# Performance work log

Measured on AMD Instinct MI355X. Metric: run time of the kernel, lower is better.

## Reference

```python
import jax, jax.numpy as jnp
import numpy as np

NEG_SLOPE = 0.2  # PyG GATConv default negative_slope
N_GRAPHS = 128


def gat_conv(x, src, dst, w, a_src, a_dst, b):
    """PyG GATConv (v1), concat=True. x:[N,F], src/dst:[E] (self-loops included),
    w:[F,H*C], a_src/a_dst:[H,C], b:[H*C]."""
    N = x.shape[0]
    H, C = a_src.shape
    h = (x @ w).reshape(N, H, C)                      # [N,H,C]
    e = (h * a_src).sum(-1)[src] + (h * a_dst).sum(-1)[dst]  # [E,H]
    e = jnp.where(e > 0, e, NEG_SLOPE * e)            # leaky_relu
    m = jax.ops.segment_max(e, dst, num_segments=N)   # per-dst softmax max
    ex = jnp.exp(e - m[dst])
    s = jax.ops.segment_sum(ex, dst, num_segments=N)
    alpha = ex / (s[dst] + 1e-16)                     # [E,H]
    out = jax.ops.segment_sum(h[src] * alpha[:, :, None], dst, num_segments=N)
    return out.reshape(N, H * C) + b


def pool(x, batch, num_graphs):
    """concat(global_mean_pool, global_max_pool)."""
    ones = jnp.ones((x.shape[0],), x.dtype)
    cnt = jax.ops.segment_sum(ones, batch, num_segments=num_graphs)
    mean = jax.ops.segment_sum(x, batch, num_segments=num_graphs) / jnp.maximum(cnt, 1.0)[:, None]
    mx = jax.ops.segment_max(x, batch, num_segments=num_graphs)
    return jnp.concatenate([mean, mx], axis=-1)


def setup_inputs() -> dict:
    key = jax.random.key(0)
    ks = jax.random.split(key, 30)
    N, E, G = 100000, 800000, N_GRAPHS
    F_in, H, C = 260, 4, 64
    HC = H * C  # 256

    def lin(k, i, o):
        return (jax.random.normal(k, (i, o), jnp.float32) * (1.0 / np.sqrt(i)))

    def att(k):
        return jax.random.normal(k, (H, C), jnp.float32) * 0.1

    return {
        "x": jax.random.normal(ks[0], (N, F_in), jnp.float32),
        "edge_index": jax.random.randint(ks[1], (2, E), 0, N),
        "batch": jnp.sort(jax.random.randint(ks[2], (N,), 0, G)),
        "gat1_w": lin(ks[3], F_in, HC), "gat1_as": att(ks[4]), "gat1_ad": att(ks[5]),
        "gat1_b": jnp.zeros((HC,), jnp.float32),
        "lin1_w": lin(ks[6], HC, C), "lin1_b": jnp.zeros((C,), jnp.float32),
        "gat2_w": lin(ks[7], C, HC), "gat2_as": att(ks[8]), "gat2_ad": att(ks[9]),
        "gat2_b": jnp.zeros((HC,), jnp.float32),
        "lin2_w": lin(ks[10], HC, C), "lin2_b": jnp.zeros((C,), jnp.float32),
        "sum_w": lin(ks[11], 4 * C, 2 * C), "sum_b": jnp.zeros((2 * C,), jnp.float32),
        "sh1_w": lin(ks[12], 2 * C, C), "sh1_b": jnp.zeros((C,), jnp.float32),
        "sh2_w": lin(ks[13], C, C), "sh2_b": jnp.zeros((C,), jnp.float32),
        "sh3_w": lin(ks[14], C, C), "sh3_b": jnp.zeros((C,), jnp.float32),
        "reg_w": lin(ks[15], C, 32), "reg_b": jnp.zeros((32,), jnp.float32),
    }


def reference(x, edge_index, batch,
              gat1_w, gat1_as, gat1_ad, gat1_b, lin1_w, lin1_b,
              gat2_w, gat2_as, gat2_ad, gat2_b, lin2_w, lin2_b,
              sum_w, sum_b, sh1_w, sh1_b, sh2_w, sh2_b, sh3_w, sh3_b,
              reg_w, reg_b):
    N = x.shape[0]
    loop = jnp.arange(N)
    src = jnp.concatenate([edge_index[0], loop])  # add_self_loops=True
    dst = jnp.concatenate([edge_index[1], loop])

    h = gat_conv(x, src, dst, gat1_w, gat1_as, gat1_ad, gat1_b)
    h = jax.nn.selu(h @ lin1_w + lin1_b)
    x1 = pool(h, batch, N_GRAPHS)                 # [G, 2C]

    h = gat_conv(h, src, dst, gat2_w, gat2_as, gat2_ad, gat2_b)
    h = jax.nn.selu(h @ lin2_w + lin2_b)
    x2 = pool(h, batch, N_GRAPHS)                 # [G, 2C]

    z = jnp.concatenate([x1, x2], axis=-1) @ sum_w + sum_b
    z = jax.nn.selu(z @ sh1_w + sh1_b)
    z = jax.nn.selu(z @ sh2_w + sh2_b)
    z = jax.nn.selu(z @ sh3_w + sh3_b)
    return z @ reg_w + reg_b                      # [G, 32]
```

## Files before the change

### kernel.cpp

```cpp
#include <hip/hip_runtime.h>
#include <hip/hip_bf16.h>
#include <cstdint>

#define NEG_SLOPE 0.2f
#define HEADS 4
#define CH 64
#define HC 256
#define F_IN 260
#define KPAD1 320
#define NGRAPH 128

typedef __attribute__((ext_vector_type(8))) short bf16x8;
typedef __attribute__((ext_vector_type(4))) float f32x4;

__device__ __forceinline__ float seluf(float x){
    const float sc=1.0507009873554805f, al=1.6732632423543772f;
    return x>0.f ? sc*x : sc*al*(__expf(x)-1.f);
}
__device__ __forceinline__ unsigned fenc(float x){
    unsigned u=__float_as_uint(x);
    return (u&0x80000000u)? ~u : (u|0x80000000u);
}
__device__ __forceinline__ float fdec(unsigned e){
    unsigned u = (e&0x80000000u)? (e&0x7fffffffu) : ~e;
    return __uint_as_float(u);
}
__device__ __forceinline__ float bf2f(unsigned short u){
    return __uint_as_float(((unsigned)u)<<16);
}
__device__ __forceinline__ unsigned short f2bf_raw(float x){
    unsigned u = __float_as_uint(x);
    unsigned rounded = u + 0x7fffu + ((u >> 16) & 1u);
    return (unsigned short)(rounded >> 16);
}
__device__ __forceinline__ void gload_lds16(const void* g, void* l){
    __builtin_amdgcn_global_load_lds(
        (const __attribute__((address_space(1))) void*)g,
        (__attribute__((address_space(3))) void*)l, 16, 0, 0);
}

__global__ void fill_u32_kernel(unsigned* p, unsigned v, int n){
    int i = blockIdx.x*blockDim.x + threadIdx.x;
    for (; i<n; i += gridDim.x*blockDim.x) p[i]=v;
}

__global__ void degree_kernel(const int* __restrict__ ei, int* __restrict__ deg, int E){
    int i = blockIdx.x*blockDim.x+threadIdx.x;
    for (; i<E; i+=gridDim.x*blockDim.x) atomicAdd(&deg[ei[E+i]], 1);
}

__global__ void scan_ph1(const int* __restrict__ deg, int* __restrict__ bsum, int N){
    __shared__ int sd[256];
    int base = blockIdx.x*1024;
    int t = threadIdx.x;
    int tot=0;
    for(int u=0;u<4;u++){ int i = base + t*4+u; tot += (i<N)? deg[i]:0; }
    sd[t]=tot; __syncthreads();
    for(int off=128; off; off>>=1){ if(t<off) sd[t]+=sd[t+off]; __syncthreads(); }
    if(t==0) bsum[blockIdx.x]=sd[0];
}
__global__ void scan_ph2(int* bsum, int nb, int* rowptr, int N, int E){
    if(threadIdx.x==0 && blockIdx.x==0){
        int run=0;
        for(int b=0;b<nb;b++){ int v=bsum[b]; bsum[b]=run; run+=v; }
        rowptr[N]=E;
    }
}
__global__ void scan_ph3(const int* __restrict__ deg, const int* __restrict__ bsum,
                         int* __restrict__ rowptr, int N){
    __shared__ int sd[256];
    int base = blockIdx.x*1024;
    int t = threadIdx.x;
    int v[4]; int tot=0;
    for(int u=0;u<4;u++){ int i=base+t*4+u; v[u] = (i<N)? deg[i]:0; tot+=v[u]; }
    sd[t]=tot; __syncthreads();
    for(int off=1; off<256; off<<=1){
        int add = (t>=off)? sd[t-off] : 0;
        __syncthreads();
        sd[t] += add;
        __syncthreads();
    }
    int pre = bsum[blockIdx.x] + ((t==0)?0: sd[t-1]);
    for(int u=0;u<4;u++){ int i=base+t*4+u; if(i<N){ rowptr[i]=pre; pre+=v[u]; } }
}

__global__ void scatter_kernel(const int* __restrict__ ei, const int* __restrict__ rowptr,
                               int* __restrict__ fil, int* __restrict__ col, int E){
    int i = blockIdx.x*blockDim.x+threadIdx.x;
    for(; i<E; i+=gridDim.x*blockDim.x){
        int s = ei[i], d = ei[E+i];
        int p = atomicAdd(&fil[d],1);
        col[rowptr[d]+p] = s;
    }
}

__global__ void cvt_x_kernel(const float* __restrict__ x, unsigned* __restrict__ xb, int N){
    int i = blockIdx.x*blockDim.x+threadIdx.x;
    int total = N*(KPAD1/2);
    for (; i<total; i+=gridDim.x*blockDim.x){
        int row = i/(KPAD1/2);
        int c2 = (i - row*(KPAD1/2))*2;
        float v0 = (c2   < F_IN) ? x[(size_t)row*F_IN + c2]   : 0.f;
        float v1 = (c2+1 < F_IN) ? x[(size_t)row*F_IN + c2+1] : 0.f;
        xb[i] = ((unsigned)f2bf_raw(v1) << 16) | f2bf_raw(v0);
    }
}

__global__ void cvt_wT_kernel(const float* __restrict__ w, __hip_bfloat16* __restrict__ wt,
                              int K, int NC, int Kpad){
    int i = blockIdx.x*blockDim.x+threadIdx.x;
    if (i >= NC*Kpad) return;
    int n = i / Kpad, k = i - n*Kpad;
    wt[i] = __float2bfloat16(k < K ? w[(size_t)k*NC + n] : 0.f);
}

template<int BN, int FS>
__global__ __launch_bounds__(512, 4) void mfma_gemm_kernel(
    const __hip_bfloat16* __restrict__ A, int Kpad,
    const __hip_bfloat16* __restrict__ Bt,
    const float* __restrict__ bias, int act,
    __hip_bfloat16* __restrict__ Cb,
    const float* __restrict__ asrc, const float* __restrict__ adst,
    float* __restrict__ ss, float* __restrict__ sdv,
    int M, int NC)
{
    constexpr int NF = BN/32;
    constexpr int WN = BN/2;
    constexpr int TP = WN + 8;
    __shared__ __align__(16) char lds[32768];

    int tid  = threadIdx.x;
    int lane = tid & 63;
    int w    = tid >> 6;
    int wr = w >> 1, wc = w & 1;
    int row0 = blockIdx.x * 128;
    int col0 = blockIdx.y * BN;
    int fr   = lane & 15;
    int koff = (lane >> 4) * 16;

    f32x4 acc[2][NF];
    #pragma unroll
    for (int i=0;i<2;i++)
        #pragma unroll
        for (int j=0;j<NF;j++) acc[i][j] = (f32x4){0.f,0.f,0.f,0.f};

    int lrow = lane >> 2;
    int lcolB = (lane & 3) * 16;
    int ktiles = Kpad >> 5;

    auto stage = [&](int kt, int pb){
        int k0b = kt*64;
        char* Asb = lds + pb*8192;
        char* Bsb = lds + 16384 + pb*(BN*64);
        {
            int gr = row0 + w*16 + lrow; if (gr > M-1) gr = M-1;
            gload_lds16((const char*)A + (size_t)gr*Kpad*2 + k0b + lcolB,
                        Asb + w*1024 + lrow*64 + lcolB);
        }
        if (w < BN/16){
            int gn = col0 + w*16 + lrow;
            gload_lds16((const char*)Bt + (size_t)gn*Kpad*2 + k0b + lcolB,
                        Bsb + w*1024 + lrow*64 + lcolB);
        }
    };

    stage(0, 0);
    __syncthreads();
    for (int kt=0; kt<ktiles; kt++){
        int pb = kt & 1;
        if (kt+1 < ktiles) stage(kt+1, pb^1);
        const char* Ab = lds + pb*8192;
        const char* Bb = lds + 16384 + pb*(BN*64);
        bf16x8 a[2], b[NF];
        a[0] = *(const bf16x8*)(Ab + (wr*32 +      fr)*64 + koff);
        a[1] = *(const bf16x8*)(Ab + (wr*32 + 16 + fr)*64 + koff);
        #pragma unroll
        for (int nt=0; nt<NF; nt++)
            b[nt] = *(const bf16x8*)(Bb + (wc*WN + nt*16 + fr)*64 + koff);
        #pragma unroll
        for (int mt=0; mt<2; mt++)
            #pragma unroll
            for (int nt=0; nt<NF; nt++)
                acc[mt][nt] = __builtin_amdgcn_mfma_f32_16x16x32_bf16(a[mt], b[nt], acc[mt][nt], 0, 0, 0);
        __syncthreads();
    }

    if (FS){
        float asv[NF], adv[NF];
        #pragma unroll
        for (int nt=0; nt<NF; nt++){
            int gc = col0 + wc*WN + nt*16 + fr;
            asv[nt] = asrc[gc];
            adv[nt] = adst[gc];
        }
        int head = (col0 + wc*WN) >> 6;
        #pragma unroll
        for (int mt=0; mt<2; mt++){
            #pragma unroll
            for (int r=0; r<4; r++){
                float ts=0.f, td=0.f;
                #pragma unroll
                for (int nt=0; nt<NF; nt++){
                    ts = fmaf(acc[mt][nt][r], asv[nt], ts);
                    td = fmaf(acc[mt][nt][r], adv[nt], td);
                }
                #pragma unroll
                for (int off=1; off<16; off<<=1){
                    ts += __shfl_xor(ts, off);
                    td += __shfl_xor(td, off);
                }
                if (fr==0){
                    int gr = row0 + wr*32 + mt*16 + (lane>>4)*4 + r;
                    if (gr < M){ ss[gr*4+head]=ts; sdv[gr*4+head]=td; }
                }
            }
        }
    }

    char* ct = lds + w*(16*TP*2);
    int c0 = col0 + wc*WN;
    #pragma unroll
    for (int mt=0; mt<2; mt++){
        #pragma unroll
        for (int nt=0; nt<NF; nt++){
            #pragma unroll
            for (int r=0; r<4; r++){
                float v = acc[mt][nt][r];
                if (bias) v += bias[c0 + nt*16 + fr];
                if (act)  v = seluf(v);
                int tr = (lane>>4)*4 + r;
                *(unsigned short*)(ct + tr*(TP*2) + (nt*16+fr)*2) = f2bf_raw(v);
            }
        }
        constexpr int CPR = WN/8;
        constexpr int RPP = 64/CPR;
        #pragma unroll
        for (int p=0; p<16/RPP; p++){
            int tr = p*RPP + lane/CPR;
            int ch = lane % CPR;
            int4 v = *(const int4*)(ct + tr*(TP*2) + ch*16);
            int gr = row0 + wr*32 + mt*16 + tr;
            if (gr < M)
                *(int4*)((char*)Cb + ((size_t)gr*NC + c0 + ch*8)*2) = v;
        }
    }
}

__global__ void softmax_prep_kernel(const float* __restrict__ ss, const float* __restrict__ sdv,
                                    const int* __restrict__ rowptr, const int* __restrict__ col,
                                    float2* __restrict__ minv, float* __restrict__ selfa, int N){
    int t = blockIdx.x*blockDim.x + threadIdx.x;
    int node = t >> 2;
    int h = t & 3;
    if (node >= N) return;
    float ad = sdv[node*4+h];
    float e0 = ss[node*4+h] + ad;
    e0 = e0>0.f ? e0 : NEG_SLOPE*e0;
    float m = e0, s = 1.f;
    int jb = rowptr[node], je = rowptr[node+1];
    for (int j=jb; j<je; j++){
        int sc = col[j];
        float e = ss[sc*4+h] + ad;
        e = e>0.f ? e : NEG_SLOPE*e;
        float mn = fmaxf(m, e);
        s = s*__expf(m-mn) + __expf(e-mn);
        m = mn;
    }
    float inv = 1.f / s;
    minv[node*4+h] = make_float2(m, inv);
    selfa[node*4+h] = __expf(e0-m)*inv;
}

__global__ void aggregate2_kernel(const __hip_bfloat16* __restrict__ h,
                                  const float* __restrict__ ss, const float* __restrict__ sdv,
                                  const float2* __restrict__ minv, const float* __restrict__ selfa,
                                  const int* __restrict__ rowptr, const int* __restrict__ col,
                                  const float* __restrict__ bias,
                                  __hip_bfloat16* __restrict__ outp, int N){
    int node = blockIdx.x*4 + (threadIdx.x>>6);
    if (node >= N) return;
    int lane = threadIdx.x & 63;
    int hh = lane >> 4;
    int c0 = (lane & 15) * 4;
    int idx = hh*64 + c0;
    const unsigned short* hp = (const unsigned short*)h;
    float ad = sdv[node*4+hh];
    float2 mi = minv[node*4+hh];
    float sa = selfa[node*4+hh];
    ushort4 hv = *(const ushort4*)(hp + (size_t)node*HC + idx);
    float a0 = sa*bf2f(hv.x), a1 = sa*bf2f(hv.y), a2 = sa*bf2f(hv.z), a3 = sa*bf2f(hv.w);
    int jb = rowptr[node], je = rowptr[node+1];
    int j = jb;
    for (; j+1 < je; j += 2){
        int sc0 = col[j], sc1 = col[j+1];
        float e0 = ss[sc0*4+hh] + ad;
        float e1 = ss[sc1*4+hh] + ad;
        e0 = e0>0.f ? e0 : NEG_SLOPE*e0;
        e1 = e1>0.f ? e1 : NEG_SLOPE*e1;
        float p0 = __expf(e0 - mi.x)*mi.y;
        float p1 = __expf(e1 - mi.x)*mi.y;
        ushort4 v0 = *(const ushort4*)(hp + (size_t)sc0*HC + idx);
        ushort4 v1 = *(const ushort4*)(hp + (size_t)sc1*HC + idx);
        a0 = fmaf(p0, bf2f(v0.x), a0); a1 = fmaf(p0, bf2f(v0.y), a1);
        a2 = fmaf(p0, bf2f(v0.z), a2); a3 = fmaf(p0, bf2f(v0.w), a3);
        a0 = fmaf(p1, bf2f(v1.x), a0); a1 = fmaf(p1, bf2f(v1.y), a1);
        a2 = fmaf(p1, bf2f(v1.z), a2); a3 = fmaf(p1, bf2f(v1.w), a3);
    }
    if (j < je){
        int sc0 = col[j];
        float e0 = ss[sc0*4+hh] + ad;
        e0 = e0>0.f ? e0 : NEG_SLOPE*e0;
        float p0 = __expf(e0 - mi.x)*mi.y;
        ushort4 v0 = *(const ushort4*)(hp + (size_t)sc0*HC + idx);
        a0 = fmaf(p0, bf2f(v0.x), a0); a1 = fmaf(p0, bf2f(v0.y), a1);
        a2 = fmaf(p0, bf2f(v0.z), a2); a3 = fmaf(p0, bf2f(v0.w), a3);
    }
    unsigned short* op = (unsigned short*)outp;
    size_t ob = (size_t)node*HC + idx;
    op[ob+0] = f2bf_raw(a0 + bias[idx+0]);
    op[ob+1] = f2bf_raw(a1 + bias[idx+1]);
    op[ob+2] = f2bf_raw(a2 + bias[idx+2]);
    op[ob+3] = f2bf_raw(a3 + bias[idx+3]);
}

__global__ void count_kernel(const int* __restrict__ batch, int* __restrict__ cnt, int N){
    int i = blockIdx.x*blockDim.x + threadIdx.x;
    if (i >= N) return;
    int lane = threadIdx.x & 63;
    int g = batch[i];
    int nfull = N & ~63;
    if (i < nfull){
        int g0 = __shfl(g, 0);
        if (__all(g==g0)){ if (lane==0) atomicAdd(&cnt[g0], 64); }
        else atomicAdd(&cnt[g], 1);
    } else {
        atomicAdd(&cnt[g], 1);
    }
}

__global__ void pool_kernel(const __hip_bfloat16* __restrict__ hs, const int* __restrict__ batch,
                            float* __restrict__ psum, unsigned* __restrict__ pmax, int N){
    int c = threadIdx.x & 63;
    int sub = threadIdx.x >> 6;
    int n0 = blockIdx.x*128 + sub*32;
    const unsigned short* hp = (const unsigned short*)hs;
    float s = 0.f, mx = -__builtin_inff();
    int cur = -1;
    for (int j=0; j<32; j++){
        int n = n0 + j;
        if (n >= N) break;
        int g = batch[n];
        if (g != cur){
            if (cur >= 0){
                atomicAdd(&psum[cur*64+c], s);
                atomicMax(&pmax[cur*64+c], fenc(mx));
            }
            cur = g; s = 0.f; mx = -__builtin_inff();
        }
        float v = bf2f(hp[(size_t)n*64 + c]);
        s += v; mx = fmaxf(mx, v);
    }
    if (cur >= 0){
        atomicAdd(&psum[cur*64+c], s);
        atomicMax(&pmax[cur*64+c], fenc(mx));
    }
}

__global__ void pool_final_kernel(const float* __restrict__ psum, const unsigned* __restrict__ pmax,
                                  const int* __restrict__ cnt, float* __restrict__ x, int G){
    int i = blockIdx.x*blockDim.x+threadIdx.x;
    if (i >= G*64) return;
    int g=i>>6, c=i&63;
    float cf = fmaxf((float)cnt[g], 1.f);
    x[g*128 + c] = psum[i]/cf;
    x[g*128 + 64 + c] = fdec(pmax[i]);
}

__global__ __launch_bounds__(128) void head_kernel(
    const float* __restrict__ x1, const float* __restrict__ x2,
    const float* __restrict__ sw, const float* __restrict__ sb,
    const float* __restrict__ w1, const float* __restrict__ b1,
    const float* __restrict__ w2, const float* __restrict__ b2,
    const float* __restrict__ w3, const float* __restrict__ b3,
    const float* __restrict__ rw, const float* __restrict__ rb,
    float* __restrict__ out)
{
    int g = blockIdx.x, t = threadIdx.x;
    __shared__ float v[256], z1[128], z2[64], z3[64], z4[64];
    v[t] = x1[g*128+t];
    v[128+t] = x2[g*128+t];
    __syncthreads();
    float a = sb[t];
    for(int k=0;k<256;k++) a = fmaf(v[k], sw[k*128+t], a);
    z1[t] = a;
    __syncthreads();
    if(t<64){
        float a2 = b1[t];
        for(int k=0;k<128;k++) a2 = fmaf(z1[k], w1[k*64+t], a2);
        z2[t] = seluf(a2);
    }
    __syncthreads();
    if(t<64){
        float a3 = b2[t];
        for(int k=0;k<64;k++) a3 = fmaf(z2[k], w2[k*64+t], a3);
        z3[t] = seluf(a3);
    }
    __syncthreads();
    if(t<64){
        float a4 = b3[t];
        for(int k=0;k<64;k++) a4 = fmaf(z3[k], w3[k*64+t], a4);
        z4[t] = seluf(a4);
    }
    __syncthreads();
    if(t<32){
        float a5 = rb[t];
        for(int k=0;k<64;k++) a5 = fmaf(z4[k], rw[k*32+t], a5);
        out[g*32+t] = a5;
    }
}

extern "C" void kernel_launch(void* const* d_in, const int* in_sizes, int n_in,
                              void* d_out, int out_size, void* d_ws, size_t ws_size,
                              hipStream_t stream)
{
    const float* x    = (const float*)d_in[0];
    const int*   ei   = (const int*)d_in[1];
    const int*   batch= (const int*)d_in[2];
    const float* g1w  = (const float*)d_in[3];
    const float* g1as = (const float*)d_in[4];
    const float* g1ad = (const float*)d_in[5];
    const float* g1b  = (const float*)d_in[6];
    const float* l1w  = (const float*)d_in[7];
    const float* l1b  = (const float*)d_in[8];
    const float* g2w  = (const float*)d_in[9];
    const float* g2as = (const float*)d_in[10];
    const float* g2ad = (const float*)d_in[11];
    const float* g2b  = (const float*)d_in[12];
    const float* l2w  = (const float*)d_in[13];
    const float* l2b  = (const float*)d_in[14];
    const float* sw   = (const float*)d_in[15];
    const float* sb   = (const float*)d_in[16];
    const float* s1w  = (const float*)d_in[17];
    const float* s1b  = (const float*)d_in[18];
    const float* s2w  = (const float*)d_in[19];
    const float* s2b  = (const float*)d_in[20];
    const float* s3w  = (const float*)d_in[21];
    const float* s3b  = (const float*)d_in[22];
    const float* rw   = (const float*)d_in[23];
    const float* rb   = (const float*)d_in[24];
    float* out = (float*)d_out;

    const int N = in_sizes[0] / F_IN;
    const int E = in_sizes[1] / 2;
    const int G = NGRAPH;

    char* ws = (char*)d_ws;
    size_t off = 0;
    auto alloc = [&](size_t bytes)->void*{
        void* p = ws + off;
        off += (bytes + 255) & ~(size_t)255;
        return p;
    };
    int* deg     = (int*)alloc((size_t)2*N*4);
    int* fil     = deg + N;
    int* rowptr  = (int*)alloc(((size_t)N+1)*4);
    int* col     = (int*)alloc((size_t)E*4);
    int* bsum    = (int*)alloc(1024);
    int* zpool   = (int*)alloc((size_t)(128 + 2*G*64)*4);
    int*   cnt = zpool;
    float* PS1 = (float*)(zpool + 128);
    float* PS2 = PS1 + G*64;
    unsigned* PM1 = (unsigned*)alloc((size_t)2*G*64*4);
    unsigned* PM2 = PM1 + G*64;
    float* X1    = (float*)alloc((size_t)G*128*4);
    float* X2    = (float*)alloc((size_t)G*128*4);
    __hip_bfloat16* Xb  = (__hip_bfloat16*)alloc((size_t)N*KPAD1*2);
    __hip_bfloat16* W1t = (__hip_bfloat16*)alloc((size_t)HC*KPAD1*2);
    __hip_bfloat16* L1t = (__hip_bfloat16*)alloc((size_t)CH*HC*2);
    __hip_bfloat16* W2t = (__hip_bfloat16*)alloc((size_t)HC*CH*2);
    __hip_bfloat16* L2t = (__hip_bfloat16*)alloc((size_t)CH*HC*2);
    __hip_bfloat16* Abf = (__hip_bfloat16*)alloc((size_t)N*HC*2);
    __hip_bfloat16* Bbf = (__hip_bfloat16*)alloc((size_t)N*HC*2);
    __hip_bfloat16* HSb = (__hip_bfloat16*)alloc((size_t)N*CH*2);
    float* SCS   = (float*)alloc((size_t)N*HEADS*4);
    float* SCD   = (float*)alloc((size_t)N*HEADS*4);
    float2* MNV  = (float2*)alloc((size_t)N*HEADS*8);
    float* SELFA = (float*)alloc((size_t)N*HEADS*4);
    (void)ws_size; (void)n_in; (void)out_size;

    const unsigned ENC_NEG_INF = 0x007FFFFFu;
    int nb = (N+1023)/1024;

    fill_u32_kernel<<<256,256,0,stream>>>((unsigned*)deg, 0u, 2*N);
    fill_u32_kernel<<<64,256,0,stream>>>((unsigned*)zpool, 0u, 128 + 2*G*64);
    fill_u32_kernel<<<64,256,0,stream>>>(PM1, ENC_NEG_INF, 2*G*64);

    degree_kernel<<<1024,256,0,stream>>>(ei, deg, E);
    scan_ph1<<<nb,256,0,stream>>>(deg, bsum, N);
    scan_ph2<<<1,64,0,stream>>>(bsum, nb, rowptr, N, E);
    scan_ph3<<<nb,256,0,stream>>>(deg, bsum, rowptr, N);
    scatter_kernel<<<1024,256,0,stream>>>(ei, rowptr, fil, col, E);

    cvt_x_kernel<<<2048,256,0,stream>>>(x, (unsigned*)Xb, N);
    cvt_wT_kernel<<<(HC*KPAD1+255)/256,256,0,stream>>>(g1w, W1t, F_IN, HC, KPAD1);
    cvt_wT_kernel<<<(CH*HC+255)/256,256,0,stream>>>(l1w, L1t, HC, CH, HC);
    cvt_wT_kernel<<<(HC*CH+255)/256,256,0,stream>>>(g2w, W2t, CH, HC, CH);
    cvt_wT_kernel<<<(CH*HC+255)/256,256,0,stream>>>(l2w, L2t, HC, CH, HC);

    int nodeBlocks = (N+3)/4;
    int prepBlocks = (N*4+255)/256;
    dim3 gA((N+127)/128, 2);
    dim3 gL((N+127)/128, 1);

    mfma_gemm_kernel<128,1><<<gA,512,0,stream>>>(Xb, KPAD1, W1t, nullptr, 0, Abf,
                                                 g1as, g1ad, SCS, SCD, N, HC);
    softmax_prep_kernel<<<prepBlocks,256,0,stream>>>(SCS, SCD, rowptr, col, MNV, SELFA, N);
    aggregate2_kernel<<<nodeBlocks,256,0,stream>>>(Abf, SCS, SCD, MNV, SELFA, rowptr, col, g1b, Bbf, N);
    mfma_gemm_kernel<64,0><<<gL,512,0,stream>>>(Bbf, HC, L1t, l1b, 1, HSb,
                                                nullptr, nullptr, nullptr, nullptr, N, CH);
    count_kernel<<<(N+255)/256,256,0,stream>>>(batch, cnt, N);
    pool_kernel<<<(N+127)/128,256,0,stream>>>(HSb, batch, PS1, PM1, N);
    pool_final_kernel<<<(G*64+255)/256,256,0,stream>>>(PS1, PM1, cnt, X1, G);

    mfma_gemm_kernel<128,1><<<gA,512,0,stream>>>(HSb, CH, W2t, nullptr, 0, Abf,
                                                 g2as, g2ad, SCS, SCD, N, HC);
    softmax_prep_kernel<<<prepBlocks,256,0,stream>>>(SCS, SCD, rowptr, col, MNV, SELFA, N);
    aggregate2_kernel<<<nodeBlocks,256,0,stream>>>(Abf, SCS, SCD, MNV, SELFA, rowptr, col, g2b, Bbf, N);
    mfma_gemm_kernel<64,0><<<gL,512,0,stream>>>(Bbf, HC, L2t, l2b, 1, HSb,
                                                nullptr, nullptr, nullptr, nullptr, N, CH);
    pool_kernel<<<(N+127)/128,256,0,stream>>>(HSb, batch, PS2, PM2, N);
    pool_final_kernel<<<(G*64+255)/256,256,0,stream>>>(PS2, PM2, cnt, X2, G);

    head_kernel<<<G,128,0,stream>>>(X1, X2, sw, sb, s1w, s1b, s2w, s2b, s3w, s3b, rw, rb, out);
}
```

Measured before the change: 524.0 us.

## Process four edges per wave in aggregate2 and shrink GEMM K padding

The aggregate2 kernel now splits each 64-lane wave into four edge slots. Each lane owns 16 contiguous channels and loads them as two 16-byte vectors, so four source rows are gathered concurrently. Partial sums are combined with cross-lane shuffles, and the output is written with wide vector stores. This is meant to raise memory-level parallelism on the irregular gathers and use wider loads and stores, at the cost of shuffle reductions and idle lanes when a node's degree is not a multiple of four. Separately, the first GEMM's K padding drops from 320 to 288 to cut wasted multiply work on the 260-wide input, which assumes 288 is still a multiple of that kernel's K tile.

```diff
diff --git a/kernel.cpp b/kernel.cpp
--- a/kernel.cpp
+++ b/kernel.cpp
@@ -7,10 +7,11 @@
 #define CH 64
 #define HC 256
 #define F_IN 260
-#define KPAD1 320
+#define KPAD1 288
 #define NGRAPH 128
 
 typedef __attribute__((ext_vector_type(8))) short bf16x8;
+typedef __attribute__((ext_vector_type(8))) unsigned short u16x8;
 typedef __attribute__((ext_vector_type(4))) float f32x4;
 
 __device__ __forceinline__ float seluf(float x){
@@ -280,47 +281,68 @@
     int node = blockIdx.x*4 + (threadIdx.x>>6);
     if (node >= N) return;
     int lane = threadIdx.x & 63;
-    int hh = lane >> 4;
-    int c0 = (lane & 15) * 4;
-    int idx = hh*64 + c0;
+    int s = lane >> 4;
+    int t = lane & 15;
+    int hh = t >> 2;
     const unsigned short* hp = (const unsigned short*)h;
+
     float ad = sdv[node*4+hh];
     float2 mi = minv[node*4+hh];
-    float sa = selfa[node*4+hh];
-    ushort4 hv = *(const ushort4*)(hp + (size_t)node*HC + idx);
-    float a0 = sa*bf2f(hv.x), a1 = sa*bf2f(hv.y), a2 = sa*bf2f(hv.z), a3 = sa*bf2f(hv.w);
+
+    float acc[16];
+    {
+        float sa = (s==0) ? selfa[node*4+hh] : 0.f;
+        const unsigned short* base = hp + (size_t)node*HC + t*16;
+        u16x8 v0 = *(const u16x8*)(base);
+        u16x8 v1 = *(const u16x8*)(base + 8);
+        #pragma unroll
+        for (int k=0;k<8;k++){
+            acc[k]   = sa * bf2f(v0[k]);
+            acc[8+k] = sa * bf2f(v1[k]);
+        }
+    }
+
     int jb = rowptr[node], je = rowptr[node+1];
-    int j = jb;
-    for (; j+1 < je; j += 2){
-        int sc0 = col[j], sc1 = col[j+1];
-        float e0 = ss[sc0*4+hh] + ad;
-        float e1 = ss[sc1*4+hh] + ad;
-        e0 = e0>0.f ? e0 : NEG_SLOPE*e0;
-        e1 = e1>0.f ? e1 : NEG_SLOPE*e1;
-        float p0 = __expf(e0 - mi.x)*mi.y;
-        float p1 = __expf(e1 - mi.x)*mi.y;
-        ushort4 v0 = *(const ushort4*)(hp + (size_t)sc0*HC + idx);
-        ushort4 v1 = *(const ushort4*)(hp + (size_t)sc1*HC + idx);
-        a0 = fmaf(p0, bf2f(v0.x), a0); a1 = fmaf(p0, bf2f(v0.y), a1);
-        a2 = fmaf(p0, bf2f(v0.z), a2); a3 = fmaf(p0, bf2f(v0.w), a3);
-        a0 = fmaf(p1, bf2f(v1.x), a0); a1 = fmaf(p1, bf2f(v1.y), a1);
-        a2 = fmaf(p1, bf2f(v1.z), a2); a3 = fmaf(p1, bf2f(v1.w), a3);
-    }
-    if (j < je){
-        int sc0 = col[j];
-        float e0 = ss[sc0*4+hh] + ad;
-        e0 = e0>0.f ? e0 : NEG_SLOPE*e0;
-        float p0 = __expf(e0 - mi.x)*mi.y;
-        ushort4 v0 = *(const ushort4*)(hp + (size_t)sc0*HC + idx);
-        a0 = fmaf(p0, bf2f(v0.x), a0); a1 = fmaf(p0, bf2f(v0.y), a1);
-        a2 = fmaf(p0, bf2f(v0.z), a2); a3 = fmaf(p0, bf2f(v0.w), a3);
-    }
-    unsigned short* op = (unsigned short*)outp;
-    size_t ob = (size_t)node*HC + idx;
-    op[ob+0] = f2bf_raw(a0 + bias[idx+0]);
-    op[ob+1] = f2bf_raw(a1 + bias[idx+1]);
-    op[ob+2] = f2bf_raw(a2 + bias[idx+2]);
-    op[ob+3] = f2bf_raw(a3 + bias[idx+3]);
+    for (int j0 = jb; j0 < je; j0 += 4){
+        int j = j0 + s;
+        float p = 0.f;
+        int sc = node;
+        if (j < je){
+            sc = col[j];
+            float e = ss[sc*4+hh] + ad;
+            e = e>0.f ? e : NEG_SLOPE*e;
+            p = __expf(e - mi.x)*mi.y;
+        }
+        const unsigned short* sb = hp + (size_t)sc*HC + t*16;
+        u16x8 v0 = *(const u16x8*)sb;
+        u16x8 v1 = *(const u16x8*)(sb + 8);
+        #pragma unroll
+        for (int k=0;k<8;k++){
+            acc[k]   = fmaf(p, bf2f(v0[k]), acc[k]);
+            acc[8+k] = fmaf(p, bf2f(v1[k]), acc[8+k]);
+        }
+    }
+
+    #pragma unroll
+    for (int k=0;k<16;k++){
+        acc[k] += __shfl_xor(acc[k], 16);
+        acc[k] += __shfl_xor(acc[k], 32);
+    }
+
+    if (s==0){
+        unsigned d[8];
+        #pragma unroll
+        for (int k=0;k<8;k++){
+            unsigned lo = f2bf_raw(acc[2*k]   + bias[t*16 + 2*k]);
+            unsigned hi = f2bf_raw(acc[2*k+1] + bias[t*16 + 2*k+1]);
+            d[k] = lo | (hi<<16);
+        }
+        unsigned short* op = (unsigned short*)outp + (size_t)node*HC + t*16;
+        int4 w0 = make_int4((int)d[0], (int)d[1], (int)d[2], (int)d[3]);
+        int4 w1 = make_int4((int)d[4], (int)d[5], (int)d[6], (int)d[7]);
+        *(int4*)op = w0;
+        *(int4*)(op + 8) = w1;
+    }
 }
 
 __global__ void count_kernel(const int* __restrict__ batch, int* __restrict__ cnt, int N){
```

Result: no change. 523.7 us (-0.1%).
